# Optimization experiments

Hardware: AMD Instinct MI355X
Metric: run time of the kernel (lower is better)

## Reference

```python
import jax, jax.numpy as jnp
import numpy as np

N, M, P = 32, 16, 32
B, T = 256, 200
STD_DYN, STD_OBS = 0.1, 0.1


def setup_inputs() -> dict:
    key = jax.random.key(0)
    k = jax.random.split(key, 6)
    Y = jax.random.normal(k[0], (B, T, P), dtype=jnp.float32)
    U = jax.random.normal(k[1], (B, T, M), dtype=jnp.float32)
    mask = jnp.ones((B, T), dtype=jnp.float32)
    # stable transition matrix
    A = 0.95 * jnp.eye(N, dtype=jnp.float32) + 0.05 * jax.random.normal(k[2], (N, N), dtype=jnp.float32) / np.sqrt(N)
    Bm = jax.random.normal(k[3], (N, M), dtype=jnp.float32) / np.sqrt(M)
    C = jax.random.normal(k[4], (P, N), dtype=jnp.float32) / np.sqrt(N)
    mu0 = jax.random.normal(k[5], (N,), dtype=jnp.float32)
    Sigma0 = jnp.eye(N, dtype=jnp.float32)
    Q = (STD_DYN ** 2) * jnp.eye(N, dtype=jnp.float32)
    R = (STD_OBS ** 2) * jnp.eye(P, dtype=jnp.float32)
    return {"Y": Y, "U": U, "mask": mask, "A": A, "Bm": Bm, "C": C,
            "mu0": mu0, "Sigma0": Sigma0, "Q": Q, "R": R}


def _sym(X):
    return 0.5 * (X + jnp.swapaxes(X, -1, -2))


def reference(Y, U, mask, A, Bm, C, mu0, Sigma0, Q, R):
    """Kalman filter forward pass (time-invariant A,B,C; Q,R diag buffers).
    Returns (mus_filt [B,T,n], Sigmas_filt [B,T,n,n], mus_pred [B,T,n],
             Sigmas_pred [B,T,n,n])."""
    Bsz = Y.shape[0]
    n = A.shape[0]
    I = jnp.eye(n, dtype=Y.dtype)

    mu_init = jnp.broadcast_to(mu0, (Bsz, n))                 # [B,n]
    Sig_init = jnp.broadcast_to(Sigma0, (Bsz, n, n))          # [B,n,n]

    def step(carry, inp):
        mu, Sigma = carry                                     # [B,n], [B,n,n]
        y_t, u_t, m_t = inp                                   # [B,p], [B,m], [B]
        # predict
        mu_pred = mu @ A.T + u_t @ Bm.T                       # [B,n]
        Sigma_pred = jnp.einsum('ij,bjk,lk->bil', A, Sigma, A) + Q
        # innovation
        r = y_t - mu_pred @ C.T                               # [B,p]
        S = _sym(jnp.einsum('ij,bjk,lk->bil', C, Sigma_pred, C) + R)  # [B,p,p]
        PCT = jnp.einsum('bij,kj->bik', Sigma_pred, C)        # [B,n,p]
        # gain: K = (solve(S, PCT^T))^T
        K = jnp.swapaxes(jnp.linalg.solve(S, jnp.swapaxes(PCT, -1, -2)), -1, -2)
        K = m_t[:, None, None] * K                            # mask missing obs
        # update (Joseph form)
        mu_new = mu_pred + jnp.einsum('bnp,bp->bn', K, r)
        I_KC = I - K @ C                                      # [B,n,n]
        Sigma_new = _sym(jnp.einsum('bij,bjk,blk->bil', I_KC, Sigma_pred, I_KC)
                         + jnp.einsum('bip,pq,bjq->bij', K, R, K))
        return (mu_new, Sigma_new), (mu_new, Sigma_new, mu_pred, Sigma_pred)

    xs = (jnp.swapaxes(Y, 0, 1), jnp.swapaxes(U, 0, 1), jnp.swapaxes(mask, 0, 1))
    _, (mf, Sf, mp, Sp) = jax.lax.scan(step, (mu_init, Sig_init), xs)
    # [T,B,...] -> [B,T,...]
    return (jnp.swapaxes(mf, 0, 1), jnp.swapaxes(Sf, 0, 1),
            jnp.swapaxes(mp, 0, 1), jnp.swapaxes(Sp, 0, 1))
```

## Files before the change

### kernel.cpp

```cpp
#include <hip/hip_runtime.h>
#include <math.h>

#define TT 200
#define ST 36
#define PA 33

__device__ __forceinline__ float rdlane(float v, int l) {
  return __int_as_float(__builtin_amdgcn_readlane(__float_as_int(v), l));
}

#if __has_builtin(__builtin_amdgcn_rsqf)
#define RSQF(x) __builtin_amdgcn_rsqf(x)
#else
#define RSQF(x) (1.0f / sqrtf(x))
#endif

__device__ __forceinline__ float4 ld4(const float* p) { return *(const float4*)p; }
__device__ __forceinline__ void st4(float* p, float4 v) { *(float4*)p = v; }

__device__ __forceinline__ float dot32r(const float* __restrict__ row, const float (&a)[32]) {
  float s0 = 0.f, s1 = 0.f;
  #pragma unroll
  for (int k = 0; k < 32; k += 8) {
    float4 v0 = ld4(row + k);
    float4 v1 = ld4(row + k + 4);
    s0 = fmaf(a[k+0], v0.x, s0); s0 = fmaf(a[k+1], v0.y, s0);
    s0 = fmaf(a[k+2], v0.z, s0); s0 = fmaf(a[k+3], v0.w, s0);
    s1 = fmaf(a[k+4], v1.x, s1); s1 = fmaf(a[k+5], v1.y, s1);
    s1 = fmaf(a[k+6], v1.z, s1); s1 = fmaf(a[k+7], v1.w, s1);
  }
  return s0 + s1;
}

__device__ __forceinline__ void dot32x2(const float* __restrict__ row,
                                        const float (&a)[32], const float (&b)[32],
                                        float& oa, float& ob) {
  float a0=0.f, a1=0.f, b0=0.f, b1=0.f;
  #pragma unroll
  for (int k = 0; k < 32; k += 8) {
    float4 v0 = ld4(row + k);
    float4 v1 = ld4(row + k + 4);
    a0 = fmaf(a[k+0], v0.x, a0); a1 = fmaf(a[k+1], v0.y, a1);
    a0 = fmaf(a[k+2], v0.z, a0); a1 = fmaf(a[k+3], v0.w, a1);
    b0 = fmaf(b[k+0], v0.x, b0); b1 = fmaf(b[k+1], v0.y, b1);
    b0 = fmaf(b[k+2], v0.z, b0); b1 = fmaf(b[k+3], v0.w, b1);
    a0 = fmaf(a[k+4], v1.x, a0); a1 = fmaf(a[k+5], v1.y, a1);
    a0 = fmaf(a[k+6], v1.z, a0); a1 = fmaf(a[k+7], v1.w, a1);
    b0 = fmaf(b[k+4], v1.x, b0); b1 = fmaf(b[k+5], v1.y, b1);
    b0 = fmaf(b[k+6], v1.z, b0); b1 = fmaf(b[k+7], v1.w, b1);
  }
  oa = a0 + a1; ob = b0 + b1;
}

__device__ __forceinline__ float dot32rr(const float* __restrict__ ra, const float* __restrict__ rb) {
  float s0 = 0.f, s1 = 0.f;
  #pragma unroll
  for (int k = 0; k < 32; k += 8) {
    float4 x0 = ld4(ra + k), x1 = ld4(ra + k + 4);
    float4 y0 = ld4(rb + k), y1 = ld4(rb + k + 4);
    s0 = fmaf(x0.x, y0.x, s0); s0 = fmaf(x0.y, y0.y, s0);
    s0 = fmaf(x0.z, y0.z, s0); s0 = fmaf(x0.w, y0.w, s0);
    s1 = fmaf(x1.x, y1.x, s1); s1 = fmaf(x1.y, y1.y, s1);
    s1 = fmaf(x1.z, y1.z, s1); s1 = fmaf(x1.w, y1.w, s1);
  }
  return s0 + s1;
}

__global__ void __launch_bounds__(512, 2) kf_kernel(
    const float* __restrict__ Yg, const float* __restrict__ Ug,
    const float* __restrict__ Mg, const float* __restrict__ Ag,
    const float* __restrict__ Bg, const float* __restrict__ Cg,
    const float* __restrict__ mu0g, const float* __restrict__ S0g,
    const float* __restrict__ Qg, const float* __restrict__ Rg,
    float* __restrict__ out, int Bsz)
{
  __shared__ __align__(16) float SIG[32*ST];
  __shared__ __align__(16) float T1[32*ST];
  __shared__ __align__(16) float SIGP[32*ST];
  __shared__ __align__(16) float T2R[32*ST];
  __shared__ __align__(16) float SR[32*ST];
  __shared__ __align__(16) float WT[33*ST];
  __shared__ __align__(16) float QL[1024], RL[1024];
  __shared__ float ALDS[32*PA], CLDS[32*PA];
  __shared__ float u_lds[16], y_lds[32], mupred[32], mu_lds[32], mlds[2];

  const int tid = threadIdx.x;
  const int q = tid >> 5;
  const int r = tid & 31;
  const int b = blockIdx.x;
  const long btB = (long)b * TT;

  const long o_Sf = (long)Bsz * TT * 32;
  const long o_mp = o_Sf + (long)Bsz * TT * 32 * 32;
  const long o_Sp = o_mp + (long)Bsz * TT * 32;

  for (int e = tid; e < 1024; e += 512) {
    int i = e >> 5, k = e & 31;
    ALDS[i*PA + k] = Ag[e];
    CLDS[i*PA + k] = Cg[e];
    QL[e] = Qg[e];
    RL[e] = Rg[e];
    SIG[i*ST + k] = S0g[e];
  }
  if (tid < 32) mu_lds[tid] = mu0g[tid];
  if (tid < 16) u_lds[tid] = Ug[btB*16 + tid];
  if (tid >= 64 && tid < 96) y_lds[tid-64] = Yg[btB*32 + (tid-64)];
  if (tid == 224) mlds[0] = Mg[btB];

  float aq0[32], aq1[32], cq0[32], cq1[32];
  #pragma unroll
  for (int k = 0; k < 32; k += 4) {
    float4 v;
    v = ld4(Ag + q*32 + k);        aq0[k]=v.x; aq0[k+1]=v.y; aq0[k+2]=v.z; aq0[k+3]=v.w;
    v = ld4(Ag + (q+16)*32 + k);   aq1[k]=v.x; aq1[k+1]=v.y; aq1[k+2]=v.z; aq1[k+3]=v.w;
    v = ld4(Cg + q*32 + k);        cq0[k]=v.x; cq0[k+1]=v.y; cq0[k+2]=v.z; cq0[k+3]=v.w;
    v = ld4(Cg + (q+16)*32 + k);   cq1[k]=v.x; cq1[k+1]=v.y; cq1[k+2]=v.z; cq1[k+3]=v.w;
  }
  __syncthreads();

  const int ro0 = q*ST + r;
  const int ro1 = (q+16)*ST + r;

  for (int t = 0; t < TT; ++t) {
    const long bt = btB + t;

    {
      float ta, tb;
      dot32x2(SIG + r*ST, aq0, aq1, ta, tb);
      T1[ro0] = ta; T1[ro1] = tb;
      if (tid < 32) {
        float s = 0.f;
        #pragma unroll
        for (int k = 0; k < 32; ++k) s = fmaf(ALDS[tid*PA + k], mu_lds[k], s);
        #pragma unroll
        for (int k = 0; k < 16; ++k) s = fmaf(Bg[tid*16 + k], u_lds[k], s);
        mupred[tid] = s;
      }
    }
    __syncthreads();

    {
      float va, vb;
      dot32x2(T1 + r*ST, aq0, aq1, va, vb);
      SIGP[ro0] = va + QL[q*32 + r];
      SIGP[ro1] = vb + QL[(q+16)*32 + r];
      if (tid < 32) {
        float s = y_lds[tid];
        #pragma unroll
        for (int k = 0; k < 32; ++k) s = fmaf(-CLDS[tid*PA + k], mupred[k], s);
        T2R[tid*ST + 32] = s;
      }
    }
    __syncthreads();

    {
      float ta, tb;
      dot32x2(SIGP + r*ST, cq0, cq1, ta, tb);
      T2R[ro0] = ta; T2R[ro1] = tb;
    }
    __syncthreads();

    {
      float sa, sb;
      dot32x2(T2R + r*ST, cq0, cq1, sa, sb);
      SR[ro0] = sa + RL[q*32 + r];
      SR[ro1] = sb + RL[(q+16)*32 + r];
    }
    __syncthreads();

    if (tid < 64) {
      int cc = tid; if (cc > 32) cc = 32;
      float w[32], rr[32];
      #pragma unroll
      for (int i = 0; i < 32; ++i) {
        w[i]  = SR[i*ST + cc];
        rr[i] = T2R[i*ST + cc];
      }
      #pragma unroll
      for (int j = 0; j < 32; ++j) {
        float d  = rdlane(w[j], j);
        float sj = RSQF(d);
        float s2 = sj * sj;
        float gw = s2 * w[j];
        float gr = s2 * rr[j];
        WT[cc*ST + j] = rr[j] * sj;
        #pragma unroll
        for (int i = j+1; i < 32; ++i) {
          float bw = rdlane(w[i], j);
          w[i]  = fmaf(-bw, gw, w[i]);
          rr[i] = fmaf(-bw, gr, rr[i]);
        }
      }
    } else {
      const int u = tid - 64;
      if (u < 256) {
        st4(out + o_Sp + bt*1024 + u*4, ld4(SIGP + (u>>3)*ST + (u&7)*4));
      } else if (t > 0) {
        const int q2 = u - 256;
        st4(out + o_Sf + (bt-1)*1024 + q2*4, ld4(SIG + (q2>>3)*ST + (q2&7)*4));
      }
      if (u < 64 && t > 0) {
        const int q2 = u + 192;
        st4(out + o_Sf + (bt-1)*1024 + q2*4, ld4(SIG + (q2>>3)*ST + (q2&7)*4));
      }
      if (tid >= 64 && tid < 96)  out[o_mp + bt*32 + (tid-64)] = mupred[tid-64];
      if (t > 0 && tid >= 96 && tid < 128) out[(bt-1)*32 + (tid-96)] = mu_lds[tid-96];
      if (t < TT-1) {
        if (tid >= 128 && tid < 144) u_lds[tid-128] = Ug[(bt+1)*16 + (tid-128)];
        if (tid >= 160 && tid < 192) y_lds[tid-160] = Yg[(bt+1)*32 + (tid-160)];
        if (tid == 200) mlds[(t+1)&1] = Mg[bt+1];
      }
    }
    __syncthreads();

    {
      const float m = mlds[t&1];
      const float coefS = fmaf(m, m, -2.f*m);
      float rv[32];
      #pragma unroll
      for (int k = 0; k < 32; k += 4) {
        float4 v = ld4(WT + r*ST + k);
        rv[k] = v.x; rv[k+1] = v.y; rv[k+2] = v.z; rv[k+3] = v.w;
      }
      float ga = dot32r(WT + q*ST, rv);
      float gb = dot32r(WT + (q+16)*ST, rv);
      SIG[ro0] = fmaf(coefS, ga, SIGP[ro0]);
      SIG[ro1] = fmaf(coefS, gb, SIGP[ro1]);
      if (tid < 32) {
        float sacc = dot32rr(WT + tid*ST, WT + 32*ST);
        mu_lds[tid] = fmaf(m, sacc, mupred[tid]);
      }
    }
    __syncthreads();
  }

  {
    const long bt = btB + TT - 1;
    if (tid < 256)
      st4(out + o_Sf + bt*1024 + tid*4, ld4(SIG + (tid>>3)*ST + (tid&7)*4));
    if (tid >= 480)
      out[bt*32 + (tid - 480)] = mu_lds[tid - 480];
  }
}

extern "C" void kernel_launch(void* const* d_in, const int* in_sizes, int n_in,
                              void* d_out, int out_size, void* d_ws, size_t ws_size,
                              hipStream_t stream) {
  const float* Y   = (const float*)d_in[0];
  const float* U   = (const float*)d_in[1];
  const float* Mk  = (const float*)d_in[2];
  const float* A   = (const float*)d_in[3];
  const float* Bm  = (const float*)d_in[4];
  const float* C   = (const float*)d_in[5];
  const float* mu0 = (const float*)d_in[6];
  const float* S0  = (const float*)d_in[7];
  const float* Q   = (const float*)d_in[8];
  const float* R   = (const float*)d_in[9];
  int Bsz = in_sizes[2] / TT;
  kf_kernel<<<Bsz, 512, 0, stream>>>(Y, U, Mk, A, Bm, C, mu0, S0, Q, R,
                                     (float*)d_out, Bsz);
}
```

Before: 1.653 ms.

## Precompute C·A products to collapse predict/innovation stages into two barriers

```diff
diff --git a/kernel.cpp b/kernel.cpp
--- a/kernel.cpp
+++ b/kernel.cpp
@@ -4,6 +4,7 @@
 #define TT 200
 #define ST 36
 #define PA 33
+#define FSTR 17
 
 __device__ __forceinline__ float rdlane(float v, int l) {
   return __int_as_float(__builtin_amdgcn_readlane(__float_as_int(v), l));
@@ -52,6 +53,25 @@
   oa = a0 + a1; ob = b0 + b1;
 }
 
+__device__ __forceinline__ void dot32x4(const float* __restrict__ row,
+    const float (&a)[32], const float (&b)[32], const float (&c)[32], const float (&d)[32],
+    float& oa, float& ob, float& oc, float& od) {
+  float sa=0.f, sb=0.f, sc=0.f, sd=0.f;
+  #pragma unroll
+  for (int k = 0; k < 32; k += 4) {
+    float4 v = ld4(row + k);
+    sa = fmaf(a[k+0], v.x, sa); sb = fmaf(b[k+0], v.x, sb);
+    sc = fmaf(c[k+0], v.x, sc); sd = fmaf(d[k+0], v.x, sd);
+    sa = fmaf(a[k+1], v.y, sa); sb = fmaf(b[k+1], v.y, sb);
+    sc = fmaf(c[k+1], v.y, sc); sd = fmaf(d[k+1], v.y, sd);
+    sa = fmaf(a[k+2], v.z, sa); sb = fmaf(b[k+2], v.z, sb);
+    sc = fmaf(c[k+2], v.z, sc); sd = fmaf(d[k+2], v.z, sd);
+    sa = fmaf(a[k+3], v.w, sa); sb = fmaf(b[k+3], v.w, sb);
+    sc = fmaf(c[k+3], v.w, sc); sd = fmaf(d[k+3], v.w, sd);
+  }
+  oa = sa; ob = sb; oc = sc; od = sd;
+}
+
 __device__ __forceinline__ float dot32rr(const float* __restrict__ ra, const float* __restrict__ rb) {
   float s0 = 0.f, s1 = 0.f;
   #pragma unroll
@@ -76,12 +96,17 @@
 {
   __shared__ __align__(16) float SIG[32*ST];
   __shared__ __align__(16) float T1[32*ST];
+  __shared__ __align__(16) float T1P[32*ST];
   __shared__ __align__(16) float SIGP[32*ST];
-  __shared__ __align__(16) float T2R[32*ST];
+  __shared__ __align__(16) float T2T[33*ST];
   __shared__ __align__(16) float SR[32*ST];
   __shared__ __align__(16) float WT[33*ST];
-  __shared__ __align__(16) float QL[1024], RL[1024];
-  __shared__ float ALDS[32*PA], CLDS[32*PA];
+  __shared__ __align__(16) float QL[1024];
+  __shared__ __align__(16) float CQT[1024];
+  __shared__ __align__(16) float EL[1024];
+  __shared__ float ALDS[32*PA];
+  __shared__ float DLDS[32*PA];
+  __shared__ float FL[32*FSTR];
   __shared__ float u_lds[16], y_lds[32], mupred[32], mu_lds[32], mlds[2];
 
   const int tid = threadIdx.x;
@@ -97,9 +122,8 @@
   for (int e = tid; e < 1024; e += 512) {
     int i = e >> 5, k = e & 31;
     ALDS[i*PA + k] = Ag[e];
-    CLDS[i*PA + k] = Cg[e];
+    SR[i*PA + k]   = Cg[e];
     QL[e] = Qg[e];
-    RL[e] = Rg[e];
     SIG[i*ST + k] = S0g[e];
   }
   if (tid < 32) mu_lds[tid] = mu0g[tid];
@@ -107,14 +131,52 @@
   if (tid >= 64 && tid < 96) y_lds[tid-64] = Yg[btB*32 + (tid-64)];
   if (tid == 224) mlds[0] = Mg[btB];
 
-  float aq0[32], aq1[32], cq0[32], cq1[32];
+  float aq0[32], aq1[32];
   #pragma unroll
   for (int k = 0; k < 32; k += 4) {
     float4 v;
-    v = ld4(Ag + q*32 + k);        aq0[k]=v.x; aq0[k+1]=v.y; aq0[k+2]=v.z; aq0[k+3]=v.w;
-    v = ld4(Ag + (q+16)*32 + k);   aq1[k]=v.x; aq1[k+1]=v.y; aq1[k+2]=v.z; aq1[k+3]=v.w;
-    v = ld4(Cg + q*32 + k);        cq0[k]=v.x; cq0[k+1]=v.y; cq0[k+2]=v.z; cq0[k+3]=v.w;
-    v = ld4(Cg + (q+16)*32 + k);   cq1[k]=v.x; cq1[k+1]=v.y; cq1[k+2]=v.z; cq1[k+3]=v.w;
+    v = ld4(Ag + q*32 + k);      aq0[k]=v.x; aq0[k+1]=v.y; aq0[k+2]=v.z; aq0[k+3]=v.w;
+    v = ld4(Ag + (q+16)*32 + k); aq1[k]=v.x; aq1[k+1]=v.y; aq1[k+2]=v.z; aq1[k+3]=v.w;
+  }
+  __syncthreads();
+
+  {
+    float d0 = 0.f, d1 = 0.f, x0 = 0.f, x1 = 0.f;
+    #pragma unroll 8
+    for (int k = 0; k < 32; ++k) {
+      float al = ALDS[k*PA + r];
+      d0 = fmaf(SR[q*PA + k],      al, d0);
+      d1 = fmaf(SR[(q+16)*PA + k], al, d1);
+      float cl = SR[r*PA + k];
+      x0 = fmaf(cl, QL[k*32 + q],      x0);
+      x1 = fmaf(cl, QL[k*32 + q + 16], x1);
+    }
+    DLDS[q*PA + r] = d0; DLDS[(q+16)*PA + r] = d1;
+    CQT[q*32 + r] = x0;  CQT[(q+16)*32 + r] = x1;
+    const int fi = tid >> 4, fj = tid & 15;
+    float f = 0.f;
+    #pragma unroll 8
+    for (int k = 0; k < 32; ++k) f = fmaf(SR[fi*PA + k], Bg[k*16 + fj], f);
+    FL[fi*FSTR + fj] = f;
+  }
+  __syncthreads();
+
+  float dq0[32], dq1[32];
+  {
+    float e0 = 0.f, e1 = 0.f;
+    #pragma unroll 8
+    for (int k = 0; k < 32; ++k) {
+      float cl = SR[r*PA + k];
+      e0 = fmaf(CQT[k*32 + q],      cl, e0);
+      e1 = fmaf(CQT[k*32 + q + 16], cl, e1);
+    }
+    EL[q*32 + r]      = e0 + Rg[q*32 + r];
+    EL[(q+16)*32 + r] = e1 + Rg[(q+16)*32 + r];
+    #pragma unroll
+    for (int k = 0; k < 32; ++k) {
+      dq0[k] = DLDS[q*PA + k];
+      dq1[k] = DLDS[(q+16)*PA + k];
+    }
   }
   __syncthreads();
 
@@ -125,9 +187,10 @@
     const long bt = btB + t;
 
     {
-      float ta, tb;
-      dot32x2(SIG + r*ST, aq0, aq1, ta, tb);
+      float ta, tb, tc, td;
+      dot32x4(SIG + r*ST, aq0, aq1, dq0, dq1, ta, tb, tc, td);
       T1[ro0] = ta; T1[ro1] = tb;
+      T1P[ro0] = tc; T1P[ro1] = td;
       if (tid < 32) {
         float s = 0.f;
         #pragma unroll
@@ -135,36 +198,29 @@
         #pragma unroll
         for (int k = 0; k < 16; ++k) s = fmaf(Bg[tid*16 + k], u_lds[k], s);
         mupred[tid] = s;
+      } else if (tid >= 64 && tid < 96) {
+        const int i = tid - 64;
+        float s = y_lds[i];
+        #pragma unroll
+        for (int k = 0; k < 32; ++k) s = fmaf(-DLDS[i*PA + k], mu_lds[k], s);
+        #pragma unroll
+        for (int k = 0; k < 16; ++k) s = fmaf(-FL[i*FSTR + k], u_lds[k], s);
+        T2T[32*ST + i] = s;
       }
     }
     __syncthreads();
 
     {
-      float va, vb;
-      dot32x2(T1 + r*ST, aq0, aq1, va, vb);
-      SIGP[ro0] = va + QL[q*32 + r];
-      SIGP[ro1] = vb + QL[(q+16)*32 + r];
-      if (tid < 32) {
-        float s = y_lds[tid];
-        #pragma unroll
-        for (int k = 0; k < 32; ++k) s = fmaf(-CLDS[tid*PA + k], mupred[k], s);
-        T2R[tid*ST + 32] = s;
-      }
-    }
-    __syncthreads();
-
-    {
-      float ta, tb;
-      dot32x2(SIGP + r*ST, cq0, cq1, ta, tb);
-      T2R[ro0] = ta; T2R[ro1] = tb;
-    }
-    __syncthreads();
-
-    {
-      float sa, sb;
-      dot32x2(T2R + r*ST, cq0, cq1, sa, sb);
-      SR[ro0] = sa + RL[q*32 + r];
-      SR[ro1] = sb + RL[(q+16)*32 + r];
+      float p0, p1;
+      dot32x2(T1 + r*ST, aq0, aq1, p0, p1);
+      float t2a, t2b, sa, sb;
+      dot32x4(T1P + r*ST, aq0, aq1, dq0, dq1, t2a, t2b, sa, sb);
+      SIGP[ro0] = p0 + QL[q*32 + r];
+      SIGP[ro1] = p1 + QL[(q+16)*32 + r];
+      T2T[ro0] = t2a + CQT[q*32 + r];
+      T2T[ro1] = t2b + CQT[(q+16)*32 + r];
+      SR[ro0] = sa + EL[q*32 + r];
+      SR[ro1] = sb + EL[(q+16)*32 + r];
     }
     __syncthreads();
 
@@ -172,9 +228,11 @@
       int cc = tid; if (cc > 32) cc = 32;
       float w[32], rr[32];
       #pragma unroll
-      for (int i = 0; i < 32; ++i) {
-        w[i]  = SR[i*ST + cc];
-        rr[i] = T2R[i*ST + cc];
+      for (int kk = 0; kk < 32; kk += 4) {
+        float4 vw = ld4(SR + cc*ST + kk);
+        w[kk] = vw.x; w[kk+1] = vw.y; w[kk+2] = vw.z; w[kk+3] = vw.w;
+        float4 vr = ld4(T2T + cc*ST + kk);
+        rr[kk] = vr.x; rr[kk+1] = vr.y; rr[kk+2] = vr.z; rr[kk+3] = vr.w;
       }
       #pragma unroll
       for (int j = 0; j < 32; ++j) {
```

New measurement: 1.607 ms (median of 2 runs). 1.03x faster.
